# Performance work log

Measured on AMD Instinct MI355X. Metric: run time of the kernel, lower is better.

Reference implementation:

```python
import jax, jax.numpy as jnp
import numpy as np

R = 4096          # proposals per image
D = 4096          # fc7 feature dim (VGG16)
C = 20            # foreground classes (VOC); logits have C+1 with background
IMG_W, IMG_H = 1216.0, 800.0
SCORE_THRESH = 0.05
NMS_THRESH = 0.5
TOPK = 100


def setup_inputs() -> dict:
    key = jax.random.key(0)
    k1, k2, k3, k4, k5 = jax.random.split(key, 5)
    x = jax.random.normal(k1, (R, D), dtype=jnp.float32)
    # build valid xyxy boxes inside the image
    xy = jax.random.uniform(k2, (R, 2)) * jnp.array([IMG_W * 0.8, IMG_H * 0.8])
    wh = jax.random.uniform(k3, (R, 2)) * jnp.array([IMG_W * 0.4, IMG_H * 0.4]) + 8.0
    boxes = jnp.concatenate([xy, xy + wh], axis=1).astype(jnp.float32)
    W_cls = (jax.random.normal(k4, (D, C + 1)) * 0.01).astype(jnp.float32)
    W_det = (jax.random.normal(k5, (D, C + 1)) * 0.01).astype(jnp.float32)
    b_cls = jnp.zeros((C + 1,), jnp.float32)
    b_det = jnp.zeros((C + 1,), jnp.float32)
    return {"x": x, "boxes": boxes, "W_cls": W_cls, "b_cls": b_cls,
            "W_det": W_det, "b_det": b_det}


def _iou_matrix(b):
    # b: (R, 4) xyxy -> (R, R) IoU
    area = (b[:, 2] - b[:, 0]) * (b[:, 3] - b[:, 1])
    lt = jnp.maximum(b[:, None, :2], b[None, :, :2])
    rb = jnp.minimum(b[:, None, 2:], b[None, :, 2:])
    wh = jnp.clip(rb - lt, 0.0)
    inter = wh[..., 0] * wh[..., 1]
    return inter / (area[:, None] + area[None, :] - inter + 1e-9)


def _nms_per_class(sc, iou):
    # sc: (R,) scores for one class; iou: (R, R) shared IoU matrix.
    # Sequential greedy NMS over score-descending order; returns bool keep mask.
    n = sc.shape[0]
    order = jnp.argsort(-sc)

    def step(supp, oi):
        kept = (sc[oi] > SCORE_THRESH) & jnp.logical_not(supp[oi])
        supp = jnp.where(kept, supp | (iou[oi] > NMS_THRESH), supp)
        return supp, kept

    _, keep_sorted = jax.lax.scan(step, jnp.zeros((n,), bool), order)
    return jnp.zeros((n,), bool).at[order].set(keep_sorted)


def reference(x, boxes, W_cls, b_cls, W_det, b_det):
    # WSDDN two-stream head: class softmax x proposal softmax
    cls_logits = x @ W_cls + b_cls                      # (R, C+1)
    det_logits = x @ W_det + b_det                      # (R, C+1)
    scores = jax.nn.softmax(cls_logits, axis=1) * jax.nn.softmax(det_logits, axis=0)
    scores = scores[:, :-1]                             # drop background column (R, C)

    # clip boxes to image (Boxes.clip)
    b = jnp.stack([jnp.clip(boxes[:, 0], 0.0, IMG_W),
                   jnp.clip(boxes[:, 1], 0.0, IMG_H),
                   jnp.clip(boxes[:, 2], 0.0, IMG_W),
                   jnp.clip(boxes[:, 3], 0.0, IMG_H)], axis=1)

    iou = _iou_matrix(b)                                # (R, R)
    # per-class NMS (batched_nms with class-agnostic boxes == independent per-class NMS)
    keep = jax.vmap(lambda s: _nms_per_class(s, iou), in_axes=1, out_axes=1)(scores)  # (R, C)

    kept_scores = scores * keep.astype(scores.dtype)
    flat = kept_scores.reshape(-1)                      # (R*C,)
    top_vals, top_idx = jax.lax.top_k(flat, TOPK)
    top_prop = top_idx // C
    top_cls = top_idx % C
    top_boxes = b[top_prop]                             # (TOPK, 4)
    return top_vals, top_boxes, top_cls
```

## Files before the change

### kernel.cpp

```cpp
#include <hip/hip_runtime.h>
#include <math.h>

#define R_N 4096
#define D_N 4096
#define C_N 20
#define IMG_W_F 1216.0f
#define IMG_H_F 800.0f
#define SCORE_TH 0.05f
#define NMS_TH 0.5f
#define TOPK_N 100

#define WF_WORDS   (128 * 2 * 64 * 4)
#define DETT_OFF   (WF_WORDS)
#define DETT_WORDS (20 * R_N)
#define DSUM_OFF   (DETT_OFF + DETT_WORDS)
#define DMAX_OFF   (DSUM_OFF + 256 * 20)

typedef short bf16x8 __attribute__((ext_vector_type(8)));
typedef float f32x4  __attribute__((ext_vector_type(4)));

__device__ __forceinline__ unsigned pk(float a, float b) {
  return __builtin_amdgcn_perm(__float_as_uint(a), __float_as_uint(b), 0x07060302u);
}
__device__ __forceinline__ float fexp(float x) { return __expf(x); }

__device__ __forceinline__ void load_clip_box(const float* boxes, int r, float* b) {
  b[0] = fminf(fmaxf(boxes[r * 4 + 0], 0.f), IMG_W_F);
  b[1] = fminf(fmaxf(boxes[r * 4 + 1], 0.f), IMG_H_F);
  b[2] = fminf(fmaxf(boxes[r * 4 + 2], 0.f), IMG_W_F);
  b[3] = fminf(fmaxf(boxes[r * 4 + 3], 0.f), IMG_H_F);
}

__global__ __launch_bounds__(256) void wT_kernel(
    const float* __restrict__ Wd, uint4* __restrict__ Wfrag) {
  const int e = blockIdx.x * 256 + threadIdx.x;
  const int l = e & 63;
  const int ct = (e >> 6) & 1;
  const int gs = e >> 7;
  const int c = ct * 16 + (l & 15);
  const int k0 = gs * 32 + (l >> 4) * 8;
  float w[8];
  if (c < 21) {
#pragma unroll
    for (int j = 0; j < 8; j++) w[j] = Wd[(size_t)(k0 + j) * 21 + c];
  } else {
#pragma unroll
    for (int j = 0; j < 8; j++) w[j] = 0.f;
  }
  uint4 v;
  v.x = pk(w[1], w[0]); v.y = pk(w[3], w[2]);
  v.z = pk(w[5], w[4]); v.w = pk(w[7], w[6]);
  Wfrag[(gs * 2 + ct) * 64 + l] = v;
}

__global__ __launch_bounds__(1024) void detgemm_kernel(
    const float* __restrict__ x, const uint4* __restrict__ Wfrag,
    float* __restrict__ detT, float* __restrict__ dsum_arr,
    float* __restrict__ dmax_arr) {
  __shared__ float red[16 * 512];
  const int t = threadIdx.x;
  const int w = t >> 6, l = t & 63;
  const int r16 = l & 15, q = l >> 4;
  const int r0 = blockIdx.x * 16;

  const float* xrow = x + (size_t)(r0 + r16) * D_N + w * 256 + q * 8;
  float4 a[16];
#pragma unroll
  for (int s = 0; s < 8; s++) {
    a[2 * s]     = *(const float4*)(xrow + s * 32);
    a[2 * s + 1] = *(const float4*)(xrow + s * 32 + 4);
  }
  __builtin_amdgcn_sched_barrier(0);

  f32x4 acc0 = {0.f, 0.f, 0.f, 0.f};
  f32x4 acc1 = {0.f, 0.f, 0.f, 0.f};
#pragma unroll
  for (int s = 0; s < 8; s++) {
    const int gs = w * 8 + s;
    union { uint4 u; bf16x8 v; } b0, b1;
    b0.u = Wfrag[(gs * 2 + 0) * 64 + l];
    b1.u = Wfrag[(gs * 2 + 1) * 64 + l];
    union { bf16x8 v; unsigned u[4]; } af;
    af.u[0] = pk(a[2 * s].y,     a[2 * s].x);
    af.u[1] = pk(a[2 * s].w,     a[2 * s].z);
    af.u[2] = pk(a[2 * s + 1].y, a[2 * s + 1].x);
    af.u[3] = pk(a[2 * s + 1].w, a[2 * s + 1].z);
    acc0 = __builtin_amdgcn_mfma_f32_16x16x32_bf16(af.v, b0.v, acc0, 0, 0, 0);
    acc1 = __builtin_amdgcn_mfma_f32_16x16x32_bf16(af.v, b1.v, acc1, 0, 0, 0);
  }

  *(f32x4*)(&red[w * 512 + (0  + r16) * 16 + q * 4]) = acc0;
  *(f32x4*)(&red[w * 512 + (16 + r16) * 16 + q * 4]) = acc1;
  __syncthreads();
  if (t < 512) {
    float v = 0.f;
#pragma unroll
    for (int w2 = 0; w2 < 16; w2++) v += red[w2 * 512 + t];
    red[t] = v;
  }
  __syncthreads();
  if (t < 320) {
    const int c = t >> 4, r = t & 15;
    float e = fexp(red[t]);
    detT[(size_t)c * R_N + r0 + r] = e;
    red[t] = e;
  }
  __syncthreads();
  if (t < 20) {
    float s = 0.f, m = 0.f;
#pragma unroll
    for (int r = 0; r < 16; r++) {
      float e = red[t * 16 + r];
      s += e; m = fmaxf(m, e);
    }
    dsum_arr[blockIdx.x * 20 + t] = s;
    dmax_arr[blockIdx.x * 20 + t] = m;
  }
}

__global__ __launch_bounds__(1024) void finale_kernel(
    const float* __restrict__ x, const float* __restrict__ Wc,
    const float* __restrict__ b_cls, const float* __restrict__ detT,
    const float* __restrict__ dsum_arr, const float* __restrict__ dmax_arr,
    const float* __restrict__ boxes, float* __restrict__ out) {
  __shared__ float ps[640];
  __shared__ float sd[20];
  __shared__ float th[20];
  __shared__ int   wl[512];
  __shared__ int   n_wl;
  __shared__ int   nc[20];
  __shared__ int   cand_r[640];
  __shared__ float cand_d[640];
  __shared__ float cand_s[640];
  __shared__ int   s_ki[512];
  __shared__ float s_ks[512];
  __shared__ float sval[TOPK_N];
  __shared__ int   sidx[TOPK_N];
  __shared__ int   s_kc;
  __shared__ int   s_total;
  const int t = threadIdx.x;

  if (t < 640) {
    const int c = t % 20, g = t / 20;
    float v = 0.f;
#pragma unroll
    for (int j = 0; j < 8; j++) v += dsum_arr[(g + 32 * j) * 20 + c];
    ps[t] = v;
  }
  if (t == 0) { n_wl = 0; s_kc = 0; }
  if (t < 20) nc[t] = 0;
  if (t < TOPK_N) { sval[t] = 0.f; sidx[t] = 0; }
  __syncthreads();
  if (t < 20) {
    float v = 0.f;
#pragma unroll
    for (int g = 0; g < 32; g++) v += ps[g * 20 + t];
    sd[t] = v;
    th[t] = SCORE_TH * v;
  }
  __syncthreads();

  if (t < 640) {
    const int c = t % 20, g = t / 20;
#pragma unroll
    for (int j = 0; j < 8; j++) {
      const int b = g + 32 * j;
      if (dmax_arr[b * 20 + c] > th[c]) {
        int p = atomicAdd(&n_wl, 1);
        if (p < 512) wl[p] = b * 20 + c;
      }
    }
  }
  __syncthreads();

  int nw = n_wl; if (nw > 512) nw = 512;
  for (int i = t; i < nw; i += 1024) {
    const int e = wl[i];
    const int b = e / 20, c = e % 20;
    const float* dp = detT + (size_t)c * R_N + b * 16;
#pragma unroll
    for (int r = 0; r < 16; r++) {
      float ex = dp[r];
      if (ex > th[c]) {
        int p = atomicAdd(&nc[c], 1);
        if (p < 32) {
          cand_r[c * 32 + p] = b * 16 + r;
          cand_d[c * 32 + p] = ex / sd[c];
        }
      }
    }
  }
  __syncthreads();
  if (t == 0) {
    int tot = 0;
#pragma unroll
    for (int c = 0; c < 20; c++) tot += (nc[c] > 32 ? 32 : nc[c]);
    s_total = tot;
  }
  __syncthreads();

  if (s_total == 0) {
    if (t < TOPK_N) {
      int prop = t / C_N;
      int cls = t - prop * C_N;
      float b[4]; load_clip_box(boxes, prop, b);
      out[t] = 0.f;
      out[TOPK_N + t * 4 + 0] = b[0];
      out[TOPK_N + t * 4 + 1] = b[1];
      out[TOPK_N + t * 4 + 2] = b[2];
      out[TOPK_N + t * 4 + 3] = b[3];
      out[TOPK_N * 5 + t] = (float)cls;
    }
    return;
  }

  for (int slot = t; slot < 640; slot += 1024) {
    const int c = slot >> 5, i = slot & 31;
    int n = nc[c]; if (n > 32) n = 32;
    if (i < n) {
      const int rr = cand_r[slot];
      float lg[21];
#pragma unroll
      for (int j = 0; j < 21; j++) lg[j] = b_cls[j];
      const float* xr = x + (size_t)rr * D_N;
      for (int k = 0; k < D_N; k++) {
        float xv = xr[k];
        const float* wr = Wc + (size_t)k * 21;
#pragma unroll
        for (int j = 0; j < 21; j++) lg[j] = fmaf(xv, wr[j], lg[j]);
      }
      float m = -1e30f;
#pragma unroll
      for (int j = 0; j < 21; j++) m = fmaxf(m, lg[j]);
      float s = 0.f;
#pragma unroll
      for (int j = 0; j < 21; j++) s += fexp(lg[j] - m);
      float p = fexp(lg[c] - m) / s;
      cand_s[slot] = p * cand_d[slot];
    }
  }
  __syncthreads();

  if (t < 20) {
    const int c = t;
    int n = nc[c]; if (n > 32) n = 32;
    float s[32]; int rr[32]; int n2 = 0;
    for (int i = 0; i < n; i++) {
      float sc = cand_s[c * 32 + i];
      if (sc > SCORE_TH) { s[n2] = sc; rr[n2] = cand_r[c * 32 + i]; n2++; }
    }
    for (int i = 1; i < n2; i++) {
      float si = s[i]; int ri = rr[i];
      int j = i - 1;
      while (j >= 0 && (s[j] < si || (s[j] == si && rr[j] > ri))) {
        s[j + 1] = s[j]; rr[j + 1] = rr[j]; j--;
      }
      s[j + 1] = si; rr[j + 1] = ri;
    }
    unsigned supp = 0;
    for (int i = 0; i < n2; i++) {
      if (supp & (1u << i)) continue;
      int g = atomicAdd(&s_kc, 1);
      if (g < 512) { s_ki[g] = rr[i] * C_N + c; s_ks[g] = s[i]; }
      float bi[4]; load_clip_box(boxes, rr[i], bi);
      float ai = (bi[2] - bi[0]) * (bi[3] - bi[1]);
      for (int j = i + 1; j < n2; j++) {
        if (supp & (1u << j)) continue;
        float bj[4]; load_clip_box(boxes, rr[j], bj);
        float aj = (bj[2] - bj[0]) * (bj[3] - bj[1]);
        float lx = fmaxf(bi[0], bj[0]), ly = fmaxf(bi[1], bj[1]);
        float rx = fminf(bi[2], bj[2]), ry = fminf(bi[3], bj[3]);
        float wdt = fmaxf(rx - lx, 0.f), hgt = fmaxf(ry - ly, 0.f);
        float inter = wdt * hgt;
        float iou = inter / (ai + aj - inter + 1e-9f);
        if (iou > NMS_TH) supp |= (1u << j);
      }
    }
  }
  __syncthreads();

  int m = s_kc; if (m > 512) m = 512;
  for (int i = t; i < m; i += 1024) {
    float si = s_ks[i]; int xi = s_ki[i];
    int rank = 0;
    for (int j = 0; j < m; j++) {
      float sj = s_ks[j]; int xj = s_ki[j];
      if (sj > si || (sj == si && xj < xi)) rank++;
    }
    if (rank < TOPK_N) { sval[rank] = si; sidx[rank] = xi; }
  }
  __syncthreads();
  if (t == 0) {
    int f = m < TOPK_N ? m : TOPK_N;
    int cur = 0;
    for (int slot = f; slot < TOPK_N; slot++) {
      for (;;) {
        bool member = false;
        for (int j = 0; j < m; j++)
          if (s_ki[j] == cur) { member = true; break; }
        if (!member) break;
        cur++;
      }
      sval[slot] = 0.f;
      sidx[slot] = cur;
      cur++;
    }
  }
  __syncthreads();
  if (t < TOPK_N) {
    int idx = sidx[t];
    int prop = idx / C_N;
    int cls = idx - prop * C_N;
    float b[4]; load_clip_box(boxes, prop, b);
    out[t] = sval[t];
    out[TOPK_N + t * 4 + 0] = b[0];
    out[TOPK_N + t * 4 + 1] = b[1];
    out[TOPK_N + t * 4 + 2] = b[2];
    out[TOPK_N + t * 4 + 3] = b[3];
    out[TOPK_N * 5 + t] = (float)cls;
  }
}

extern "C" void kernel_launch(void* const* d_in, const int* in_sizes, int n_in,
                              void* d_out, int out_size, void* d_ws, size_t ws_size,
                              hipStream_t stream) {
  const float* x     = (const float*)d_in[0];
  const float* boxes = (const float*)d_in[1];
  const float* W_cls = (const float*)d_in[2];
  const float* b_cls = (const float*)d_in[3];
  const float* W_det = (const float*)d_in[4];

  float* out      = (float*)d_out;
  float* ws       = (float*)d_ws;
  uint4* Wfrag    = (uint4*)ws;
  float* detT     = ws + DETT_OFF;
  float* dsum_arr = ws + DSUM_OFF;
  float* dmax_arr = ws + DMAX_OFF;

  wT_kernel     <<<64,  256,  0, stream>>>(W_det, Wfrag);
  detgemm_kernel<<<256, 1024, 0, stream>>>(x, Wfrag, detT, dsum_arr, dmax_arr);
  finale_kernel <<<1,   1024, 0, stream>>>(x, W_cls, b_cls, detT,
                                           dsum_arr, dmax_arr, boxes, out);
}
```

Baseline: 112.5 us.

## Stage x rows through double-buffered LDS with direct global-to-LDS loads

Replaces per-lane register loads of strided x fragments in the det GEMM with global_load_lds copies. Each wave streams one whole row slice contiguously into a swizzled, double-buffered LDS tile, and the MFMA fragments are then read back from LDS. The aim is fully coalesced row reads and overlap of the next chunk's load with the current chunk's MFMAs. In exchange it doubles LDS use and adds a block-wide barrier per iteration. It also relies on the XOR swizzle being consistent between writes and reads.

```diff
diff --git a/kernel.cpp b/kernel.cpp
--- a/kernel.cpp
+++ b/kernel.cpp
@@ -23,6 +23,12 @@
   return __builtin_amdgcn_perm(__float_as_uint(a), __float_as_uint(b), 0x07060302u);
 }
 __device__ __forceinline__ float fexp(float x) { return __expf(x); }
+
+__device__ __forceinline__ void g2lds16(const float* g, float* l) {
+  __builtin_amdgcn_global_load_lds(
+      (const __attribute__((address_space(1))) unsigned*)g,
+      (__attribute__((address_space(3))) unsigned*)l, 16, 0, 0);
+}
 
 __device__ __forceinline__ void load_clip_box(const float* boxes, int r, float* b) {
   b[0] = fminf(fmaxf(boxes[r * 4 + 0], 0.f), IMG_W_F);
@@ -57,38 +63,52 @@
     const float* __restrict__ x, const uint4* __restrict__ Wfrag,
     float* __restrict__ detT, float* __restrict__ dsum_arr,
     float* __restrict__ dmax_arr) {
-  __shared__ float red[16 * 512];
+  __shared__ float lds[2][16 * 512];
   const int t = threadIdx.x;
   const int w = t >> 6, l = t & 63;
   const int r16 = l & 15, q = l >> 4;
   const int r0 = blockIdx.x * 16;
-
-  const float* xrow = x + (size_t)(r0 + r16) * D_N + w * 256 + q * 8;
-  float4 a[16];
-#pragma unroll
-  for (int s = 0; s < 8; s++) {
-    a[2 * s]     = *(const float4*)(xrow + s * 32);
-    a[2 * s + 1] = *(const float4*)(xrow + s * 32 + 4);
-  }
-  __builtin_amdgcn_sched_barrier(0);
+  const int swz = w & 7;
+  const int rs = r16 & 7;
+
+  const float* xw = x + (size_t)(r0 + w) * D_N;
+
+#define STAGE(buf, s)                                                  \
+  do {                                                                 \
+    g2lds16(xw + (s) * 512 + ((l ^ swz) << 2),        &lds[buf][w * 512]);       \
+    g2lds16(xw + (s) * 512 + (((64 | l) ^ swz) << 2), &lds[buf][w * 512 + 256]); \
+  } while (0)
+
+  STAGE(0, 0);
+  __syncthreads();
 
   f32x4 acc0 = {0.f, 0.f, 0.f, 0.f};
   f32x4 acc1 = {0.f, 0.f, 0.f, 0.f};
-#pragma unroll
-  for (int s = 0; s < 8; s++) {
-    const int gs = w * 8 + s;
+  int cur = 0;
+#pragma unroll
+  for (int s = 0; s < 8; ++s) {
+    if (s < 7) STAGE(cur ^ 1, s + 1);
+    const int gs = s * 16 + w;
     union { uint4 u; bf16x8 v; } b0, b1;
     b0.u = Wfrag[(gs * 2 + 0) * 64 + l];
     b1.u = Wfrag[(gs * 2 + 1) * 64 + l];
+    const float* bb = &lds[cur][r16 * 512];
+    const int c0 = w * 8 + q * 2;
+    float4 v0 = *(const float4*)(bb + ((c0)     ^ rs) * 4);
+    float4 v1 = *(const float4*)(bb + ((c0 + 1) ^ rs) * 4);
     union { bf16x8 v; unsigned u[4]; } af;
-    af.u[0] = pk(a[2 * s].y,     a[2 * s].x);
-    af.u[1] = pk(a[2 * s].w,     a[2 * s].z);
-    af.u[2] = pk(a[2 * s + 1].y, a[2 * s + 1].x);
-    af.u[3] = pk(a[2 * s + 1].w, a[2 * s + 1].z);
+    af.u[0] = pk(v0.y, v0.x);
+    af.u[1] = pk(v0.w, v0.z);
+    af.u[2] = pk(v1.y, v1.x);
+    af.u[3] = pk(v1.w, v1.z);
     acc0 = __builtin_amdgcn_mfma_f32_16x16x32_bf16(af.v, b0.v, acc0, 0, 0, 0);
     acc1 = __builtin_amdgcn_mfma_f32_16x16x32_bf16(af.v, b1.v, acc1, 0, 0, 0);
-  }
-
+    __syncthreads();
+    cur ^= 1;
+  }
+#undef STAGE
+
+  float* red = lds[0];
   *(f32x4*)(&red[w * 512 + (0  + r16) * 16 + q * 4]) = acc0;
   *(f32x4*)(&red[w * 512 + (16 + r16) * 16 + q * 4]) = acc1;
   __syncthreads();
```

Result: no change. 112.6 us (+0.0%).
